# Kernel optimization log

Hardware: AMD Instinct MI355X
Metric: run time of the kernel (lower is better)

## Reference

```python
import jax, jax.numpy as jnp
import numpy as np

N_NODES = 50000
N_EDGES = 800000
N_FEAT = 128
N_GRAPHS = 512
OUT_DIM = 128


def gcn_conv(x, W, b, src, dst, ew, n):
    """PyG GCNConv: h = x @ W; add self-loops (weight 1); symmetric norm
    D^-1/2 A D^-1/2 with edge weights; scatter-add messages src->dst; + bias."""
    h = x @ W  # [n, out]
    loop = jnp.arange(n)
    s = jnp.concatenate([src, loop])
    d = jnp.concatenate([dst, loop])
    w = jnp.concatenate([ew, jnp.ones((n,), x.dtype)])
    deg = jax.ops.segment_sum(w, d, num_segments=n)
    dinv = jnp.where(deg > 0, jax.lax.rsqrt(deg), 0.0)
    norm = dinv[s] * w * dinv[d]  # [E+n]
    out = jax.ops.segment_sum(h[s] * norm[:, None], d, num_segments=n)
    return out + b


def setup_inputs() -> dict:
    key = jax.random.key(0)
    ks = jax.random.split(key, 12)
    F = N_FEAT
    x = jax.random.normal(ks[0], (N_NODES, F), jnp.float32)
    edge_index = jax.random.randint(ks[1], (2, N_EDGES), 0, N_NODES, jnp.int64)
    edge_attr = jax.random.uniform(ks[2], (N_EDGES,), jnp.float32)
    # deterministic sorted graph assignment -> no empty graphs (avoids -inf in max pool)
    batch = (jnp.arange(N_NODES, dtype=jnp.int64) * N_GRAPHS) // N_NODES
    def lin(k, fi, fo):
        s = 1.0 / np.sqrt(fi)
        return jax.random.uniform(k, (fi, fo), jnp.float32, -s, s)
    return {
        "x": x, "edge_attr": edge_attr,
        "W1": lin(ks[3], F, F), "b1": jnp.zeros((F,), jnp.float32),
        "W2": lin(ks[4], F, 2 * F), "b2": jnp.zeros((2 * F,), jnp.float32),
        "W3": lin(ks[5], 2 * F, 4 * F), "b3": jnp.zeros((4 * F,), jnp.float32),
        "Wf1": lin(ks[6], 4 * F, 1024), "bf1": jnp.zeros((1024,), jnp.float32),
        "Wf2": lin(ks[7], 1024, OUT_DIM), "bf2": jnp.zeros((OUT_DIM,), jnp.float32),
        "edge_index": edge_index, "batch": batch,
    }


def reference(x, edge_attr, W1, b1, W2, b2, W3, b3, Wf1, bf1, Wf2, bf2,
              edge_index, batch):
    n = x.shape[0]
    src, dst = edge_index[0], edge_index[1]
    h = jax.nn.relu(gcn_conv(x, W1, b1, src, dst, edge_attr, n))
    h = jax.nn.relu(gcn_conv(h, W2, b2, src, dst, edge_attr, n))
    h = jax.nn.relu(gcn_conv(h, W3, b3, src, dst, edge_attr, n))
    # global max pool over nodes per graph
    g = jax.ops.segment_max(h, batch, num_segments=N_GRAPHS)  # [G, 4F]
    g = jax.nn.relu(g @ Wf1 + bf1)
    # dropout is identity in eval mode
    out = g @ Wf2 + bf2
    return out
```

## Files before the change

kernel.cpp:

```cpp
#include <hip/hip_runtime.h>

#define NNODES 50000
#define NEDGES 800000
#define NGRAPH 512
#define DCAP 64

typedef short bf16x8 __attribute__((ext_vector_type(8)));
typedef unsigned short u16x8 __attribute__((ext_vector_type(8)));
typedef float f32x4 __attribute__((ext_vector_type(4)));
typedef unsigned long long u64;

static __device__ __forceinline__ float b2f(unsigned short u) {
    return __uint_as_float(((unsigned)u) << 16);
}
static __device__ __forceinline__ unsigned short f2b(float f) {
    unsigned u = __float_as_uint(f);
    unsigned r = (u + 0x7fffu + ((u >> 16) & 1u)) >> 16;
    return (unsigned short)r;
}

static __device__ __forceinline__ void accum8(float (&acc)[8], float c, uint4 v) {
    unsigned w[4] = {v.x, v.y, v.z, v.w};
    #pragma unroll
    for (int i = 0; i < 4; ++i) {
        acc[2 * i]     += c * __uint_as_float(w[i] << 16);
        acc[2 * i + 1] += c * __uint_as_float(w[i] & 0xffff0000u);
    }
}

__global__ void k_setup(u64* deg_cnt, int* gp) {
    int i = blockIdx.x * 256 + threadIdx.x;
    if (i < NNODES) deg_cnt[i] = (u64)(1u << 24);
    if (i < NGRAPH * 512) gp[i] = 0;
}

__global__ __launch_bounds__(256) void k_count(const int4* __restrict__ ei_s,
                                               const int4* __restrict__ ei_d,
                                               const float4* __restrict__ ew4,
                                               u64* deg_cnt,
                                               unsigned* __restrict__ edges) {
    int t = blockIdx.x * 256 + threadIdx.x;
    if (t >= NEDGES / 4) return;
    int4 ss = ei_s[t];
    int4 dd = ei_d[t];
    float4 ww = ew4[t];
    int s[4] = {ss.x, ss.y, ss.z, ss.w};
    int d[4] = {dd.x, dd.y, dd.z, dd.w};
    float w[4] = {ww.x, ww.y, ww.z, ww.w};
    int slot[4];
    #pragma unroll
    for (int u = 0; u < 4; ++u) {
        unsigned fixed = __float2uint_rn(w[u] * 16777216.0f);
        u64 old = atomicAdd(&deg_cnt[d[u]], ((u64)1 << 32) | fixed);
        slot[u] = (int)(old >> 32);
        if (slot[u] > DCAP - 1) slot[u] = DCAP - 1;
    }
    #pragma unroll
    for (int u = 0; u < 4; ++u)
        edges[((unsigned)d[u] << 6) | slot[u]] = ((unsigned)f2b(w[u]) << 16) | (unsigned)s[u];
}

__global__ void k_prep(const u64* __restrict__ deg_cnt, float* __restrict__ dinv) {
    int i = blockIdx.x * 256 + threadIdx.x;
    if (i < NNODES)
        dinv[i] = rsqrtf((float)(unsigned)(deg_cnt[i] & 0xffffffffull) * 5.9604645e-8f);
}

__global__ void k_wt_all(const float* __restrict__ W1, const float* __restrict__ W2,
                         const float* __restrict__ W3, const float* __restrict__ Wf1,
                         const float* __restrict__ Wf2,
                         unsigned short* __restrict__ T1, unsigned short* __restrict__ T2,
                         unsigned short* __restrict__ T3, unsigned short* __restrict__ Tf1,
                         unsigned short* __restrict__ Tf2) {
    int i = blockIdx.x * 256 + threadIdx.x;
    const float* W; unsigned short* T; int K, ns;
    if (i < 16384)        { W = W1;  T = T1;  K = 128;  ns = 7;  }
    else if (i < 49152)   { W = W2;  T = T2;  K = 128;  ns = 8;  i -= 16384; }
    else if (i < 180224)  { W = W3;  T = T3;  K = 256;  ns = 9;  i -= 49152; }
    else if (i < 704512)  { W = Wf1; T = Tf1; K = 512;  ns = 10; i -= 180224; }
    else if (i < 835584)  { W = Wf2; T = Tf2; K = 1024; ns = 7;  i -= 704512; }
    else return;
    int k = i >> ns, n = i & ((1 << ns) - 1);
    T[(size_t)n * K + k] = f2b(W[i]);
}

__global__ void k_cvt4(const float* __restrict__ X, const float* __restrict__ dinv,
                       unsigned short* __restrict__ Y, int n4) {
    int i = blockIdx.x * 256 + threadIdx.x;
    if (i < n4) {
        float4 v = ((const float4*)X)[i];
        float d = dinv[i >> 5];
        uint2 o;
        o.x = (unsigned)f2b(v.x * d) | ((unsigned)f2b(v.y * d) << 16);
        o.y = (unsigned)f2b(v.z * d) | ((unsigned)f2b(v.w * d) << 16);
        ((uint2*)Y)[i] = o;
    }
}

template <int F>
__global__ __launch_bounds__(256) void k_aggregate(const unsigned short* __restrict__ X,
                                                   const u64* __restrict__ deg_cnt,
                                                   const unsigned* __restrict__ edges,
                                                   const float* __restrict__ dinv,
                                                   unsigned short* __restrict__ Z) {
    constexpr int LPR = F / 8;
    constexpr int GRP = 64 / LPR;
    constexpr int STEP = GRP * 2;
    const int wave = threadIdx.x >> 6, lane = threadIdx.x & 63;
    const int node = blockIdx.x * 4 + wave;
    if (node >= NNODES) return;
    const int sub = lane & (LPR - 1);
    const int grp = lane / LPR;
    const int fo = sub * 8;
    const unsigned short* Xf = X + fo;
    const float di = dinv[node];
    const int cnt = (int)(deg_cnt[node] >> 32);
    const unsigned* erow = edges + ((unsigned)node << 6);

    const uint4 selfv = *(const uint4*)(Xf + (size_t)node * F);

    float acc[8] = {};

    const int e0 = grp;
    const int nb = (cnt + STEP - 1) / STEP;

    unsigned pa0 = 0, pb0 = 0, pa1 = 0, pb1 = 0;
    uint4 va0 = {}, vb0 = {};
    if (nb > 0) {
        int ea = e0, eb = e0 + GRP;
        pa0 = (ea < cnt) ? erow[ea] : 0u;
        pb0 = (eb < cnt) ? erow[eb] : 0u;
        va0 = *(const uint4*)(Xf + (size_t)(pa0 & 0xffffu) * F);
        vb0 = *(const uint4*)(Xf + (size_t)(pb0 & 0xffffu) * F);
        if (nb > 1) {
            int ea1 = e0 + STEP, eb1 = ea1 + GRP;
            pa1 = (ea1 < cnt) ? erow[ea1] : 0u;
            pb1 = (eb1 < cnt) ? erow[eb1] : 0u;
        }
    }
    for (int p = 0; p < nb; ++p) {
        uint4 va1 = {}, vb1 = {};
        unsigned pa2 = 0, pb2 = 0;
        if (p + 1 < nb) {
            va1 = *(const uint4*)(Xf + (size_t)(pa1 & 0xffffu) * F);
            vb1 = *(const uint4*)(Xf + (size_t)(pb1 & 0xffffu) * F);
            if (p + 2 < nb) {
                int ea = e0 + (p + 2) * STEP, eb = ea + GRP;
                pa2 = (ea < cnt) ? erow[ea] : 0u;
                pb2 = (eb < cnt) ? erow[eb] : 0u;
            }
        }
        accum8(acc, b2f((unsigned short)(pa0 >> 16)), va0);
        accum8(acc, b2f((unsigned short)(pb0 >> 16)), vb0);
        pa0 = pa1; pb0 = pb1; va0 = va1; vb0 = vb1;
        pa1 = pa2; pb1 = pb2;
    }

    #pragma unroll
    for (int j = 0; j < 8; ++j) {
        if constexpr (GRP == 4) acc[j] += __shfl_xor(acc[j], 16, 64);
        acc[j] += __shfl_xor(acc[j], 32, 64);
    }

    if (grp == 0) {
        unsigned w[4] = {selfv.x, selfv.y, selfv.z, selfv.w};
        unsigned o[4];
        #pragma unroll
        for (int i = 0; i < 4; ++i) {
            float s0 = __uint_as_float(w[i] << 16);
            float s1 = __uint_as_float(w[i] & 0xffff0000u);
            unsigned short c0 = f2b(di * (acc[2 * i] + s0));
            unsigned short c1 = f2b(di * (acc[2 * i + 1] + s1));
            o[i] = (unsigned)c0 | ((unsigned)c1 << 16);
        }
        uint4 ov; ov.x = o[0]; ov.y = o[1]; ov.z = o[2]; ov.w = o[3];
        *(uint4*)(Z + (size_t)node * F + fo) = ov;
    }
}

template <int CMODE, int AFP>
__global__ __launch_bounds__(256) void k_gemm_mfma(const void* __restrict__ Av,
                                                   const unsigned short* __restrict__ WT,
                                                   const float* __restrict__ bias,
                                                   void* __restrict__ Cv,
                                                   const int* __restrict__ batch,
                                                   int* __restrict__ gp,
                                                   const float* __restrict__ rscale,
                                                   int M, int N, int K) {
    constexpr int LDK = 40;
    __shared__ unsigned short As[64 * LDK];
    __shared__ unsigned short Bs[128 * LDK];
    const int tid = threadIdx.x;
    const int m0 = blockIdx.y * 64, n0 = blockIdx.x * 128;
    const int wave = tid >> 6, lane = tid & 63;
    const int wm = (wave >> 1) * 32;
    const int wn = (wave & 1) * 64;
    const int quad = lane >> 4, mrow = lane & 15;

    const int ar = tid >> 2;
    const int ak = (tid & 3) * 8;
    const bool arow_ok = (m0 + ar) < M;
    const size_t aoff = (size_t)(m0 + ar) * K + ak;
    const unsigned short* Bg0 = WT + (size_t)(n0 + ar) * K + ak;
    const unsigned short* Bg1 = WT + (size_t)(n0 + ar + 64) * K + ak;

    f32x4 acc[2][4] = {};

    for (int k0 = 0; k0 < K; k0 += 32) {
        u16x8 av = {};
        if (arow_ok) {
            if constexpr (AFP) {
                const float* Af = (const float*)Av + aoff + k0;
                float4 f0 = *(const float4*)Af;
                float4 f1 = *(const float4*)(Af + 4);
                av[0] = (short)f2b(f0.x); av[1] = (short)f2b(f0.y);
                av[2] = (short)f2b(f0.z); av[3] = (short)f2b(f0.w);
                av[4] = (short)f2b(f1.x); av[5] = (short)f2b(f1.y);
                av[6] = (short)f2b(f1.z); av[7] = (short)f2b(f1.w);
            } else {
                av = *(const u16x8*)((const unsigned short*)Av + aoff + k0);
            }
        }
        u16x8 bv0 = *(const u16x8*)(Bg0 + k0);
        u16x8 bv1 = *(const u16x8*)(Bg1 + k0);
        *(u16x8*)&As[ar * LDK + ak] = av;
        *(u16x8*)&Bs[ar * LDK + ak] = bv0;
        *(u16x8*)&Bs[(ar + 64) * LDK + ak] = bv1;
        __syncthreads();
        bf16x8 af[2], bf[4];
        #pragma unroll
        for (int mt = 0; mt < 2; ++mt)
            af[mt] = *(const bf16x8*)&As[(wm + mt * 16 + mrow) * LDK + quad * 8];
        #pragma unroll
        for (int nt = 0; nt < 4; ++nt)
            bf[nt] = *(const bf16x8*)&Bs[(wn + nt * 16 + mrow) * LDK + quad * 8];
        #pragma unroll
        for (int mt = 0; mt < 2; ++mt)
            #pragma unroll
            for (int nt = 0; nt < 4; ++nt)
                acc[mt][nt] = __builtin_amdgcn_mfma_f32_16x16x32_bf16(af[mt], bf[nt], acc[mt][nt], 0, 0, 0);
        __syncthreads();
    }

    float bn[4];
    #pragma unroll
    for (int nt = 0; nt < 4; ++nt) bn[nt] = bias[n0 + wn + nt * 16 + mrow];

    if constexpr (CMODE == 0) {
        unsigned short* C = (unsigned short*)Cv;
        #pragma unroll
        for (int mt = 0; mt < 2; ++mt) {
            #pragma unroll
            for (int r = 0; r < 4; ++r) {
                int row = m0 + wm + mt * 16 + quad * 4 + r;
                if (row < M) {
                    float rs = rscale ? rscale[row] : 1.0f;
                    #pragma unroll
                    for (int nt = 0; nt < 4; ++nt) {
                        float v = fmaxf(acc[mt][nt][r] + bn[nt], 0.f) * rs;
                        C[(size_t)row * N + n0 + wn + nt * 16 + mrow] = f2b(v);
                    }
                }
            }
        }
    } else if constexpr (CMODE == 1) {
        float* C = (float*)Cv;
        #pragma unroll
        for (int mt = 0; mt < 2; ++mt) {
            #pragma unroll
            for (int r = 0; r < 4; ++r) {
                int row = m0 + wm + mt * 16 + quad * 4 + r;
                if (row < M) {
                    #pragma unroll
                    for (int nt = 0; nt < 4; ++nt)
                        C[(size_t)row * N + n0 + wn + nt * 16 + mrow] = acc[mt][nt][r] + bn[nt];
                }
            }
        }
    } else {
        __shared__ float pools[2][2][128];
        const int g0 = batch[m0];
        int last = m0 + 63; if (last >= M) last = M - 1;
        const int gl = batch[last];
        int  gid[8];
        bool rok[8];
        #pragma unroll
        for (int mt = 0; mt < 2; ++mt)
            #pragma unroll
            for (int r = 0; r < 4; ++r) {
                int row = m0 + wm + mt * 16 + quad * 4 + r;
                rok[mt * 4 + r] = row < M;
                gid[mt * 4 + r] = (row < M) ? batch[row] : -1;
            }
        #pragma unroll
        for (int nt = 0; nt < 4; ++nt) {
            float v0 = 0.f, v1 = 0.f;
            #pragma unroll
            for (int mt = 0; mt < 2; ++mt)
                #pragma unroll
                for (int r = 0; r < 4; ++r) {
                    if (rok[mt * 4 + r]) {
                        float v = fmaxf(acc[mt][nt][r] + bn[nt], 0.f);
                        if (gid[mt * 4 + r] == g0) v0 = fmaxf(v0, v);
                        else v1 = fmaxf(v1, v);
                    }
                }
            v0 = fmaxf(v0, __shfl_xor(v0, 16, 64));
            v0 = fmaxf(v0, __shfl_xor(v0, 32, 64));
            v1 = fmaxf(v1, __shfl_xor(v1, 16, 64));
            v1 = fmaxf(v1, __shfl_xor(v1, 32, 64));
            if (quad == 0) {
                int c = wn + nt * 16 + mrow;
                pools[wm >> 5][0][c] = v0;
                pools[wm >> 5][1][c] = v1;
            }
        }
        __syncthreads();
        int c = tid & 127, gi = tid >> 7;
        float v = fmaxf(pools[0][gi][c], pools[1][gi][c]);
        int g = gi ? gl : g0;
        if (gi == 0 || gl != g0)
            atomicMax(&gp[(size_t)g * N + n0 + c], __float_as_int(v));
    }
}

extern "C" void kernel_launch(void* const* d_in, const int* in_sizes, int n_in,
                              void* d_out, int out_size, void* d_ws, size_t ws_size,
                              hipStream_t stream) {
    const float* x   = (const float*)d_in[0];
    const float* ew  = (const float*)d_in[1];
    const float* W1  = (const float*)d_in[2];
    const float* b1  = (const float*)d_in[3];
    const float* W2  = (const float*)d_in[4];
    const float* b2  = (const float*)d_in[5];
    const float* W3  = (const float*)d_in[6];
    const float* b3  = (const float*)d_in[7];
    const float* Wf1 = (const float*)d_in[8];
    const float* bf1 = (const float*)d_in[9];
    const float* Wf2 = (const float*)d_in[10];
    const float* bf2 = (const float*)d_in[11];
    const int* ei    = (const int*)d_in[12];
    const int* batch = (const int*)d_in[13];
    float* out = (float*)d_out;
    (void)in_sizes; (void)n_in; (void)out_size; (void)ws_size;

    char* p = (char*)d_ws;
    auto alloc = [&](size_t bytes) -> char* {
        char* r = p;
        p += (bytes + 255) & ~(size_t)255;
        return r;
    };
    const int nbN = (NNODES + 255) / 256;
    u64*   deg_cnt = (u64*)alloc((size_t)NNODES * 8);
    float* dinv   = (float*)alloc((size_t)NNODES * 4);
    unsigned* edges = (unsigned*)alloc((size_t)NNODES * DCAP * 4);
    int*   gp     = (int*)  alloc((size_t)NGRAPH * 512 * 4);
    unsigned short* f1   = (unsigned short*)alloc((size_t)NGRAPH * 1024 * 2);
    unsigned short* wt1  = (unsigned short*)alloc((size_t)128 * 128 * 2);
    unsigned short* wt2  = (unsigned short*)alloc((size_t)256 * 128 * 2);
    unsigned short* wt3  = (unsigned short*)alloc((size_t)512 * 256 * 2);
    unsigned short* wtf1 = (unsigned short*)alloc((size_t)1024 * 512 * 2);
    unsigned short* wtf2 = (unsigned short*)alloc((size_t)128 * 1024 * 2);
    unsigned short* bufA = (unsigned short*)alloc((size_t)NNODES * 256 * 2);
    unsigned short* bufB = (unsigned short*)alloc((size_t)NNODES * 256 * 2);
    unsigned short* x16  = bufB;

    const int MB = (NNODES + 63) / 64;
    const int AGG = (NNODES + 3) / 4;

    k_setup<<<1024, 256, 0, stream>>>(deg_cnt, gp);
    k_count<<<(NEDGES / 4 + 255) / 256, 256, 0, stream>>>(
        (const int4*)ei, (const int4*)(ei + NEDGES), (const float4*)ew, deg_cnt, edges);
    k_prep<<<nbN, 256, 0, stream>>>(deg_cnt, dinv);
    k_wt_all<<<(835584 + 255) / 256, 256, 0, stream>>>(W1, W2, W3, Wf1, Wf2,
                                                       wt1, wt2, wt3, wtf1, wtf2);
    k_cvt4<<<(NNODES * 32 + 255) / 256, 256, 0, stream>>>(x, dinv, x16, NNODES * 32);

    k_aggregate<128><<<AGG, 256, 0, stream>>>(x16, deg_cnt, edges, dinv, bufA);
    k_gemm_mfma<0, 0><<<dim3(1, MB), 256, 0, stream>>>(bufA, wt1, b1, bufB, batch, nullptr, dinv, NNODES, 128, 128);
    k_aggregate<128><<<AGG, 256, 0, stream>>>(bufB, deg_cnt, edges, dinv, bufA);
    k_gemm_mfma<0, 0><<<dim3(2, MB), 256, 0, stream>>>(bufA, wt2, b2, bufB, batch, nullptr, dinv, NNODES, 256, 128);
    k_aggregate<256><<<AGG, 256, 0, stream>>>(bufB, deg_cnt, edges, dinv, bufA);
    k_gemm_mfma<2, 0><<<dim3(4, MB), 256, 0, stream>>>(bufA, wt3, b3, nullptr, batch, gp, nullptr, NNODES, 512, 256);

    k_gemm_mfma<0, 1><<<dim3(8, NGRAPH / 64), 256, 0, stream>>>(gp, wtf1, bf1, f1, batch, nullptr, nullptr, NGRAPH, 1024, 512);
    k_gemm_mfma<1, 0><<<dim3(1, NGRAPH / 64), 256, 0, stream>>>(f1, wtf2, bf2, out, batch, nullptr, nullptr, NGRAPH, 128, 1024);
}
```

Baseline: 371.1 us.

## Split aggregation feature dimension into 64-wide slices across blocks

The aggregation kernel now splits each node's feature vector into 64-column slices, each handled by a separate block. Every wave uses 8 lanes per row and 8 edge groups, so more edges are processed in parallel per node and the grid grows by 2x or 4x. This aims to raise memory-level parallelism for the random neighbour gathers. In exchange, edge indices and weights are re-read once per slice and an extra shuffle reduction step is added.

```diff
diff --git a/kernel.cpp b/kernel.cpp
--- a/kernel.cpp
+++ b/kernel.cpp
@@ -97,21 +97,21 @@
     }
 }
 
-template <int F>
+template <int F, int S>
 __global__ __launch_bounds__(256) void k_aggregate(const unsigned short* __restrict__ X,
                                                    const u64* __restrict__ deg_cnt,
                                                    const unsigned* __restrict__ edges,
                                                    const float* __restrict__ dinv,
                                                    unsigned short* __restrict__ Z) {
-    constexpr int LPR = F / 8;
-    constexpr int GRP = 64 / LPR;
-    constexpr int STEP = GRP * 2;
+    const int bid = blockIdx.x;
+    const int slice = bid & (S - 1);
+    const int chunk = bid / S;
     const int wave = threadIdx.x >> 6, lane = threadIdx.x & 63;
-    const int node = blockIdx.x * 4 + wave;
+    const int node = chunk * 4 + wave;
     if (node >= NNODES) return;
-    const int sub = lane & (LPR - 1);
-    const int grp = lane / LPR;
-    const int fo = sub * 8;
+    const int sub = lane & 7;
+    const int grp = lane >> 3;
+    const int fo = slice * 64 + sub * 8;
     const unsigned short* Xf = X + fo;
     const float di = dinv[node];
     const int cnt = (int)(deg_cnt[node] >> 32);
@@ -120,22 +120,19 @@
     const uint4 selfv = *(const uint4*)(Xf + (size_t)node * F);
 
     float acc[8] = {};
-
     const int e0 = grp;
-    const int nb = (cnt + STEP - 1) / STEP;
+    const int nb = (cnt + 15) / 16;
 
     unsigned pa0 = 0, pb0 = 0, pa1 = 0, pb1 = 0;
     uint4 va0 = {}, vb0 = {};
     if (nb > 0) {
-        int ea = e0, eb = e0 + GRP;
-        pa0 = (ea < cnt) ? erow[ea] : 0u;
-        pb0 = (eb < cnt) ? erow[eb] : 0u;
+        pa0 = (e0 < cnt) ? erow[e0] : 0u;
+        pb0 = (e0 + 8 < cnt) ? erow[e0 + 8] : 0u;
         va0 = *(const uint4*)(Xf + (size_t)(pa0 & 0xffffu) * F);
         vb0 = *(const uint4*)(Xf + (size_t)(pb0 & 0xffffu) * F);
         if (nb > 1) {
-            int ea1 = e0 + STEP, eb1 = ea1 + GRP;
-            pa1 = (ea1 < cnt) ? erow[ea1] : 0u;
-            pb1 = (eb1 < cnt) ? erow[eb1] : 0u;
+            pa1 = (e0 + 16 < cnt) ? erow[e0 + 16] : 0u;
+            pb1 = (e0 + 24 < cnt) ? erow[e0 + 24] : 0u;
         }
     }
     for (int p = 0; p < nb; ++p) {
@@ -145,9 +142,9 @@
             va1 = *(const uint4*)(Xf + (size_t)(pa1 & 0xffffu) * F);
             vb1 = *(const uint4*)(Xf + (size_t)(pb1 & 0xffffu) * F);
             if (p + 2 < nb) {
-                int ea = e0 + (p + 2) * STEP, eb = ea + GRP;
+                int ea = e0 + (p + 2) * 16;
                 pa2 = (ea < cnt) ? erow[ea] : 0u;
-                pb2 = (eb < cnt) ? erow[eb] : 0u;
+                pb2 = (ea + 8 < cnt) ? erow[ea + 8] : 0u;
             }
         }
         accum8(acc, b2f((unsigned short)(pa0 >> 16)), va0);
@@ -158,7 +155,8 @@
 
     #pragma unroll
     for (int j = 0; j < 8; ++j) {
-        if constexpr (GRP == 4) acc[j] += __shfl_xor(acc[j], 16, 64);
+        acc[j] += __shfl_xor(acc[j], 8, 64);
+        acc[j] += __shfl_xor(acc[j], 16, 64);
         acc[j] += __shfl_xor(acc[j], 32, 64);
     }
 
@@ -366,7 +364,7 @@
     unsigned short* x16  = bufB;
 
     const int MB = (NNODES + 63) / 64;
-    const int AGG = (NNODES + 3) / 4;
+    const int CH = (NNODES + 3) / 4;
 
     k_setup<<<1024, 256, 0, stream>>>(deg_cnt, gp);
     k_count<<<(NEDGES / 4 + 255) / 256, 256, 0, stream>>>(
@@ -376,11 +374,11 @@
                                                        wt1, wt2, wt3, wtf1, wtf2);
     k_cvt4<<<(NNODES * 32 + 255) / 256, 256, 0, stream>>>(x, dinv, x16, NNODES * 32);
 
-    k_aggregate<128><<<AGG, 256, 0, stream>>>(x16, deg_cnt, edges, dinv, bufA);
+    k_aggregate<128, 2><<<CH * 2, 256, 0, stream>>>(x16, deg_cnt, edges, dinv, bufA);
     k_gemm_mfma<0, 0><<<dim3(1, MB), 256, 0, stream>>>(bufA, wt1, b1, bufB, batch, nullptr, dinv, NNODES, 128, 128);
-    k_aggregate<128><<<AGG, 256, 0, stream>>>(bufB, deg_cnt, edges, dinv, bufA);
+    k_aggregate<128, 2><<<CH * 2, 256, 0, stream>>>(bufB, deg_cnt, edges, dinv, bufA);
     k_gemm_mfma<0, 0><<<dim3(2, MB), 256, 0, stream>>>(bufA, wt2, b2, bufB, batch, nullptr, dinv, NNODES, 256, 128);
-    k_aggregate<256><<<AGG, 256, 0, stream>>>(bufB, deg_cnt, edges, dinv, bufA);
+    k_aggregate<256, 4><<<CH * 4, 256, 0, stream>>>(bufB, deg_cnt, edges, dinv, bufA);
     k_gemm_mfma<2, 0><<<dim3(4, MB), 256, 0, stream>>>(bufA, wt3, b3, nullptr, batch, gp, nullptr, NNODES, 512, 256);
 
     k_gemm_mfma<0, 1><<<dim3(8, NGRAPH / 64), 256, 0, stream>>>(gp, wtf1, bf1, f1, batch, nullptr, nullptr, NGRAPH, 1024, 512);
```

Result: slower. 402.2 us (+8.4%).

## Add dedicated full-width GEMM+maxpool kernel for layer 3

Applied to the files above, without the earlier changes.

Replaces the generic layer-3 GEMM with pooling epilogue (64x128 tiles, grid 4 across N) by a dedicated kernel with 512 threads that computes all 512 output columns for a 32-row tile. Each A tile is now loaded once per block instead of four times, and the shared-memory pool reduction is replaced by direct per-wave atomicMax. In exchange, the block holds a larger B tile in LDS, issues more atomics per block, and the grid has twice as many row blocks.

```diff
diff --git a/kernel.cpp b/kernel.cpp
--- a/kernel.cpp
+++ b/kernel.cpp
@@ -183,8 +183,6 @@
                                                    const unsigned short* __restrict__ WT,
                                                    const float* __restrict__ bias,
                                                    void* __restrict__ Cv,
-                                                   const int* __restrict__ batch,
-                                                   int* __restrict__ gp,
                                                    const float* __restrict__ rscale,
                                                    int M, int N, int K) {
     constexpr int LDK = 40;
@@ -263,7 +261,7 @@
                 }
             }
         }
-    } else if constexpr (CMODE == 1) {
+    } else {
         float* C = (float*)Cv;
         #pragma unroll
         for (int mt = 0; mt < 2; ++mt) {
@@ -277,50 +275,91 @@
                 }
             }
         }
-    } else {
-        __shared__ float pools[2][2][128];
-        const int g0 = batch[m0];
-        int last = m0 + 63; if (last >= M) last = M - 1;
-        const int gl = batch[last];
-        int  gid[8];
-        bool rok[8];
+    }
+}
+
+__global__ __launch_bounds__(512) void k_gemm_pool512(const unsigned short* __restrict__ A,
+                                                      const unsigned short* __restrict__ WT,
+                                                      const float* __restrict__ bias,
+                                                      const int* __restrict__ batch,
+                                                      int* __restrict__ gp,
+                                                      int M) {
+    constexpr int LDK = 40;
+    __shared__ unsigned short As[32 * LDK];
+    __shared__ unsigned short Bs[512 * LDK];
+    const int tid = threadIdx.x;
+    const int m0 = blockIdx.y * 32;
+    const int wave = tid >> 6, lane = tid & 63;
+    const int wn = wave * 64;
+    const int quad = lane >> 4, mrow = lane & 15;
+    const int r4 = tid >> 2, c8 = (tid & 3) * 8;
+
+    f32x4 acc[2][4] = {};
+
+    for (int k0 = 0; k0 < 256; k0 += 32) {
+        u16x8 av = {};
+        if (tid < 128) {
+            int row = m0 + r4;
+            if (row < M) av = *(const u16x8*)(A + (size_t)row * 256 + k0 + c8);
+        }
+        u16x8 bv[4];
+        #pragma unroll
+        for (int rep = 0; rep < 4; ++rep)
+            bv[rep] = *(const u16x8*)(WT + (size_t)(rep * 128 + r4) * 256 + k0 + c8);
+        if (tid < 128) *(u16x8*)&As[r4 * LDK + c8] = av;
+        #pragma unroll
+        for (int rep = 0; rep < 4; ++rep)
+            *(u16x8*)&Bs[(rep * 128 + r4) * LDK + c8] = bv[rep];
+        __syncthreads();
+        bf16x8 af[2], bf[4];
+        #pragma unroll
+        for (int mt = 0; mt < 2; ++mt)
+            af[mt] = *(const bf16x8*)&As[(mt * 16 + mrow) * LDK + quad * 8];
+        #pragma unroll
+        for (int nt = 0; nt < 4; ++nt)
+            bf[nt] = *(const bf16x8*)&Bs[(wn + nt * 16 + mrow) * LDK + quad * 8];
         #pragma unroll
         for (int mt = 0; mt < 2; ++mt)
             #pragma unroll
-            for (int r = 0; r < 4; ++r) {
-                int row = m0 + wm + mt * 16 + quad * 4 + r;
-                rok[mt * 4 + r] = row < M;
-                gid[mt * 4 + r] = (row < M) ? batch[row] : -1;
-            }
-        #pragma unroll
-        for (int nt = 0; nt < 4; ++nt) {
-            float v0 = 0.f, v1 = 0.f;
+            for (int nt = 0; nt < 4; ++nt)
+                acc[mt][nt] = __builtin_amdgcn_mfma_f32_16x16x32_bf16(af[mt], bf[nt], acc[mt][nt], 0, 0, 0);
+        __syncthreads();
+    }
+
+    const int g0 = batch[m0];
+    int last = m0 + 31; if (last >= M) last = M - 1;
+    const int gl = batch[last];
+    bool rok[8]; int gid[8];
+    #pragma unroll
+    for (int mt = 0; mt < 2; ++mt)
+        #pragma unroll
+        for (int r = 0; r < 4; ++r) {
+            int row = m0 + mt * 16 + quad * 4 + r;
+            rok[mt * 4 + r] = row < M;
+            gid[mt * 4 + r] = (row < M) ? batch[row] : -1;
+        }
+    #pragma unroll
+    for (int nt = 0; nt < 4; ++nt) {
+        float bn = bias[wn + nt * 16 + mrow];
+        float v0 = 0.f, v1 = 0.f;
+        #pragma unroll
+        for (int mt = 0; mt < 2; ++mt)
             #pragma unroll
-            for (int mt = 0; mt < 2; ++mt)
-                #pragma unroll
-                for (int r = 0; r < 4; ++r) {
-                    if (rok[mt * 4 + r]) {
-                        float v = fmaxf(acc[mt][nt][r] + bn[nt], 0.f);
-                        if (gid[mt * 4 + r] == g0) v0 = fmaxf(v0, v);
-                        else v1 = fmaxf(v1, v);
-                    }
+            for (int r = 0; r < 4; ++r)
+                if (rok[mt * 4 + r]) {
+                    float v = fmaxf(acc[mt][nt][r] + bn, 0.f);
+                    if (gid[mt * 4 + r] == g0) v0 = fmaxf(v0, v);
+                    else v1 = fmaxf(v1, v);
                 }
-            v0 = fmaxf(v0, __shfl_xor(v0, 16, 64));
-            v0 = fmaxf(v0, __shfl_xor(v0, 32, 64));
-            v1 = fmaxf(v1, __shfl_xor(v1, 16, 64));
-            v1 = fmaxf(v1, __shfl_xor(v1, 32, 64));
-            if (quad == 0) {
-                int c = wn + nt * 16 + mrow;
-                pools[wm >> 5][0][c] = v0;
-                pools[wm >> 5][1][c] = v1;
-            }
-        }
-        __syncthreads();
-        int c = tid & 127, gi = tid >> 7;
-        float v = fmaxf(pools[0][gi][c], pools[1][gi][c]);
-        int g = gi ? gl : g0;
-        if (gi == 0 || gl != g0)
-            atomicMax(&gp[(size_t)g * N + n0 + c], __float_as_int(v));
+        v0 = fmaxf(v0, __shfl_xor(v0, 16, 64));
+        v0 = fmaxf(v0, __shfl_xor(v0, 32, 64));
+        v1 = fmaxf(v1, __shfl_xor(v1, 16, 64));
+        v1 = fmaxf(v1, __shfl_xor(v1, 32, 64));
+        if (quad == 0) {
+            int c = wn + nt * 16 + mrow;
+            atomicMax(&gp[(size_t)g0 * 512 + c], __float_as_int(v0));
+            if (gl != g0) atomicMax(&gp[(size_t)gl * 512 + c], __float_as_int(v1));
+        }
     }
 }
 
@@ -366,6 +405,7 @@
     unsigned short* x16  = bufB;
 
     const int MB = (NNODES + 63) / 64;
+    const int MBP = (NNODES + 31) / 32;
     const int AGG = (NNODES + 3) / 4;
 
     k_setup<<<1024, 256, 0, stream>>>(deg_cnt, gp);
@@ -377,12 +417,12 @@
     k_cvt4<<<(NNODES * 32 + 255) / 256, 256, 0, stream>>>(x, dinv, x16, NNODES * 32);
 
     k_aggregate<128><<<AGG, 256, 0, stream>>>(x16, deg_cnt, edges, dinv, bufA);
-    k_gemm_mfma<0, 0><<<dim3(1, MB), 256, 0, stream>>>(bufA, wt1, b1, bufB, batch, nullptr, dinv, NNODES, 128, 128);
+    k_gemm_mfma<0, 0><<<dim3(1, MB), 256, 0, stream>>>(bufA, wt1, b1, bufB, dinv, NNODES, 128, 128);
     k_aggregate<128><<<AGG, 256, 0, stream>>>(bufB, deg_cnt, edges, dinv, bufA);
-    k_gemm_mfma<0, 0><<<dim3(2, MB), 256, 0, stream>>>(bufA, wt2, b2, bufB, batch, nullptr, dinv, NNODES, 256, 128);
+    k_gemm_mfma<0, 0><<<dim3(2, MB), 256, 0, stream>>>(bufA, wt2, b2, bufB, dinv, NNODES, 256, 128);
     k_aggregate<256><<<AGG, 256, 0, stream>>>(bufB, deg_cnt, edges, dinv, bufA);
-    k_gemm_mfma<2, 0><<<dim3(4, MB), 256, 0, stream>>>(bufA, wt3, b3, nullptr, batch, gp, nullptr, NNODES, 512, 256);
-
-    k_gemm_mfma<0, 1><<<dim3(8, NGRAPH / 64), 256, 0, stream>>>(gp, wtf1, bf1, f1, batch, nullptr, nullptr, NGRAPH, 1024, 512);
-    k_gemm_mfma<1, 0><<<dim3(1, NGRAPH / 64), 256, 0, stream>>>(f1, wtf2, bf2, out, batch, nullptr, nullptr, NGRAPH, 128, 1024);
-}
+    k_gemm_pool512<<<dim3(1, MBP), 512, 0, stream>>>(bufA, wt3, b3, batch, gp, NNODES);
+
+    k_gemm_mfma<0, 1><<<dim3(8, NGRAPH / 64), 256, 0, stream>>>(gp, wtf1, bf1, f1, nullptr, NGRAPH, 1024, 512);
+    k_gemm_mfma<1, 0><<<dim3(1, NGRAPH / 64), 256, 0, stream>>>(f1, wtf2, bf2, out, nullptr, NGRAPH, 128, 1024);
+}
```

Measured after the change: 385.2 us. 3.8% more time.
